# Optimization experiments

Hardware: AMD Instinct MI355X
Metric: run time of the kernel (lower is better)

Reference implementation:

```python
import jax, jax.numpy as jnp
import numpy as np

K = 9  # 3x3 kernel taps

def _conv3x3(x, w, b):
    # standard 3x3 conv, stride 1, pad 1, NCHW
    y = jax.lax.conv_general_dilated(x, w, (1, 1), [(1, 1), (1, 1)],
                                     dimension_numbers=('NCHW', 'OIHW', 'NCHW'))
    return y + b[None, :, None, None]

def setup_inputs() -> dict:
    key = jax.random.key(0)
    ks = jax.random.split(key, 4)
    B, C, Cout, H, W = 2, 256, 256, 128, 128
    x = jax.random.normal(ks[0], (B, C, H, W), jnp.float32)
    w_off = jax.random.normal(ks[1], (3 * K, C, 3, 3), jnp.float32) * 0.01
    b_off = jnp.zeros((3 * K,), jnp.float32)
    weight = jax.random.normal(ks[2], (Cout, C, 3, 3), jnp.float32) * (1.0 / np.sqrt(K * C))
    bias = jnp.zeros((Cout,), jnp.float32)
    gamma = jnp.ones((Cout,), jnp.float32)
    beta = jnp.zeros((Cout,), jnp.float32)
    return {"x": x, "w_off": w_off, "b_off": b_off, "weight": weight,
            "bias": bias, "gamma": gamma, "beta": beta}

def _deform_gather(x, off_y, off_x, mask):
    # x: [B,C,H,W]; off_y/off_x/mask: [B,K,H,W]
    # returns modulated bilinear samples [B,C,K,H,W]
    B, C, H, W = x.shape
    kh = (jnp.arange(K, dtype=x.dtype) // 3).reshape(1, K, 1, 1)
    kw = (jnp.arange(K, dtype=x.dtype) % 3).reshape(1, K, 1, 1)
    # sampling position per tap: base - pad + tap*dilation + learned offset
    py = jnp.arange(H, dtype=x.dtype).reshape(1, 1, H, 1) - 1.0 + kh + off_y
    px = jnp.arange(W, dtype=x.dtype).reshape(1, 1, 1, W) - 1.0 + kw + off_x
    y0 = jnp.floor(py); x0 = jnp.floor(px)
    wy1 = py - y0; wx1 = px - x0
    xf = x.reshape(B, C, H * W)
    def corner(iy, ix, wgt):
        valid = (iy >= 0) & (iy <= H - 1) & (ix >= 0) & (ix <= W - 1)
        iyc = jnp.clip(iy, 0, H - 1).astype(jnp.int32)
        ixc = jnp.clip(ix, 0, W - 1).astype(jnp.int32)
        lin = (iyc * W + ixc).reshape(B, 1, K * H * W)
        g = jnp.take_along_axis(xf, lin, axis=2).reshape(B, C, K, H, W)
        return g * jnp.where(valid, wgt, 0.0)[:, None]  # zero outside borders
    val = (corner(y0,     x0,     (1 - wy1) * (1 - wx1))
         + corner(y0,     x0 + 1, (1 - wy1) * wx1)
         + corner(y0 + 1, x0,     wy1 * (1 - wx1))
         + corner(y0 + 1, x0 + 1, wy1 * wx1))
    return val * mask[:, None]

def reference(x, w_off, b_off, weight, bias, gamma, beta):
    B, C, H, W = x.shape
    om = _conv3x3(x, w_off, b_off)  # [B, 3K, H, W]
    off_y = om[:, :K]
    off_x = om[:, K:2 * K]
    m = jax.nn.sigmoid(om[:, 2 * K:])  # modulation mask
    sampled = _deform_gather(x, off_y, off_x, m)  # [B,C,K,H,W]
    Cout = weight.shape[0]
    y = jnp.einsum('bckhw,ock->bohw', sampled, weight.reshape(Cout, C, K))
    y = y + bias[None, :, None, None]
    # BatchNorm2d (training-mode batch stats, eps=1e-5) + ReLU
    mu = jnp.mean(y, axis=(0, 2, 3), keepdims=True)
    var = jnp.var(y, axis=(0, 2, 3), keepdims=True)
    yn = (y - mu) * jax.lax.rsqrt(var + 1e-5)
    return jax.nn.relu(yn * gamma[None, :, None, None] + beta[None, :, None, None])
```

## Files before the change

kernel.cpp:

```cpp
#include <hip/hip_runtime.h>
#include <hip/hip_fp16.h>
#include <math.h>

#define HW 16384
#define Cc 256
#define CO 256

typedef unsigned short u16;
typedef unsigned int   u32;
typedef __attribute__((ext_vector_type(8))) _Float16 f16x8;
typedef __attribute__((ext_vector_type(4))) float f32x4;

__device__ __forceinline__ u16 f2h(float f) {
    return __half_as_ushort(__float2half(f));
}

__global__ void k_prep(const float* __restrict__ w, const float* __restrict__ wof,
                       u16* __restrict__ wfr, u16* __restrict__ wofr) {
    int id = blockIdx.x * 256 + threadIdx.x;
    if (id < 589824) {
        int i    = id & 7;
        int lane = (id >> 3) & 63;
        int fb   = id >> 9;
        int k32  = fb % 72;
        int ot   = fb / 72;
        int o  = ot * 16 + (lane & 15);
        int K  = k32 * 32 + (lane >> 4) * 8 + i;
        int kt = K >> 8;
        int c  = K & 255;
        wfr[id] = f2h(w[((size_t)o * 256 + c) * 9 + kt]);
    } else if (id < 663552) {
        int id2  = id - 589824;
        int i    = id2 & 7;
        int lane = (id2 >> 3) & 63;
        int fb   = id2 >> 9;
        int k32  = fb % 72;
        int mt   = fb / 72;
        int o  = mt * 16 + (lane & 15);
        int K  = k32 * 32 + (lane >> 4) * 8 + i;
        int t  = K >> 8;
        int c  = K & 255;
        float v = (o < 27) ? wof[((size_t)o * 256 + c) * 9 + t] : 0.0f;
        wofr[id2] = f2h(v);
    }
}

__global__ __launch_bounds__(256) void k_xt(const float* __restrict__ x, u16* __restrict__ Xt) {
    const int tid = threadIdx.x;
    const int bid = blockIdx.x;
    const int hw0 = (bid & 255) * 64;
    const int b   = bid >> 8;
    const int hwl = tid & 63;
    const int cg  = tid >> 6;
    const int hw  = hw0 + hwl;
    const float* xb = x + ((size_t)b << 22);
    u16* dst = Xt + (((size_t)b << 14) + hw) * 256 + cg * 64;
    #pragma unroll
    for (int oct = 0; oct < 8; ++oct) {
        int c0 = cg * 64 + oct * 8;
        u32 pk[4];
        #pragma unroll
        for (int q = 0; q < 4; ++q) {
            float v0 = xb[((size_t)(c0 + 2 * q) << 14) + hw];
            float v1 = xb[((size_t)(c0 + 2 * q + 1) << 14) + hw];
            pk[q] = (u32)f2h(v0) | ((u32)f2h(v1) << 16);
        }
        *(uint4*)(dst + oct * 8) = make_uint4(pk[0], pk[1], pk[2], pk[3]);
    }
}

__global__ __launch_bounds__(256) void k_offmfma(const u16* __restrict__ Xt,
                                                 const u16* __restrict__ wofr,
                                                 const float* __restrict__ bof,
                                                 float* __restrict__ om) {
    const int tid  = threadIdx.x;
    const int wid  = tid >> 6;
    const int lane = tid & 63;
    const int bid  = blockIdx.x;
    const int wq   = bid & 1;
    const int h    = (bid >> 1) & 127;
    const int b    = bid >> 8;

    const int lr = lane & 15;
    const int lg = lane >> 4;
    const int w  = wq * 64 + wid * 16 + lr;

    f32x4 acc0 = (f32x4)0.0f, acc1 = (f32x4)0.0f;
    const u16* XtB = Xt + (((size_t)b << 14) << 8);

    for (int t = 0; t < 9; ++t) {
        int dh = t / 3 - 1;
        int dw = t % 3 - 1;
        int hh = h + dh;
        int ww = w + dw;
        bool valid = (hh >= 0) && (hh < 128) && (ww >= 0) && (ww < 128);
        int hc = min(max(hh, 0), 127);
        int wc = min(max(ww, 0), 127);
        const u16* xrow = XtB + ((size_t)(hc * 128 + wc) << 8) + lg * 8;
        #pragma unroll
        for (int c32 = 0; c32 < 8; ++c32) {
            int k32 = t * 8 + c32;
            f16x8 bv = *(const f16x8*)(xrow + c32 * 32);
            if (!valid) bv = (f16x8)0;
            f16x8 a0 = *(const f16x8*)(wofr + (((size_t)k32 * 64 + lane) << 3));
            f16x8 a1 = *(const f16x8*)(wofr + ((((size_t)(72 + k32)) * 64 + lane) << 3));
            acc0 = __builtin_amdgcn_mfma_f32_16x16x32_f16(a0, bv, acc0, 0, 0, 0);
            acc1 = __builtin_amdgcn_mfma_f32_16x16x32_f16(a1, bv, acc1, 0, 0, 0);
        }
    }

    float* omb = om + ((size_t)b * 27 << 14) + h * 128 + w;
    #pragma unroll
    for (int j = 0; j < 4; ++j) {
        int o = lg * 4 + j;
        omb[(size_t)o << 14] = acc0[j] + bof[o];
        int o1 = 16 + lg * 4 + j;
        if (o1 < 27) omb[(size_t)o1 << 14] = acc1[j] + bof[o1];
    }
}

__global__ __launch_bounds__(512) void k_sgemm(const u16* __restrict__ Xt,
                                               const float* __restrict__ om,
                                               const u16* __restrict__ wfr,
                                               const float* __restrict__ bias,
                                               u16* __restrict__ y,
                                               float* __restrict__ psum) {
    __shared__ int4    soff[9][64];
    __shared__ __half2 swt2[9][64][4];
    __shared__ __align__(16) u16 Blds[2][4096];

    const int tid  = threadIdx.x;
    const int wid  = tid >> 6;
    const int lane = tid & 63;
    const int bid  = ((blockIdx.x & 7) << 6) | (blockIdx.x >> 3);
    const int p0   = bid * 64;
    const int b    = p0 >> 14;
    const int hwb  = p0 & 16383;

    for (int e = tid; e < 576; e += 512) {
        int t = e >> 6, j = e & 63;
        int hw = hwb + j;
        int h = hw >> 7, wc = hw & 127;
        const size_t ob = (size_t)b * 27 * HW;
        float oy = om[ob + (size_t)t * HW + hw];
        float ox = om[ob + (size_t)(9 + t) * HW + hw];
        float mv = om[ob + (size_t)(18 + t) * HW + hw];
        mv = 1.0f / (1.0f + expf(-mv));
        float py = (float)h - 1.0f + (float)(t / 3) + oy;
        float px = (float)wc - 1.0f + (float)(t % 3) + ox;
        float y0f = floorf(py), x0f = floorf(px);
        float wy = py - y0f, wx = px - x0f;
        int iy = (int)y0f, ix = (int)x0f;
        float w4[4] = {(1.0f - wy) * (1.0f - wx), (1.0f - wy) * wx,
                       wy * (1.0f - wx),          wy * wx};
        const int dy[4] = {0, 0, 1, 1};
        const int dx[4] = {0, 1, 0, 1};
        int of[4];
        #pragma unroll
        for (int r = 0; r < 4; ++r) {
            int yy = iy + dy[r], xx = ix + dx[r];
            bool v = (yy >= 0) && (yy <= 127) && (xx >= 0) && (xx <= 127);
            int yc = min(max(yy, 0), 127);
            int xc = min(max(xx, 0), 127);
            of[r] = yc * 128 + xc;
            swt2[t][j][r] = __float2half2_rn(v ? w4[r] * mv : 0.0f);
        }
        soff[t][j] = make_int4(of[0], of[1], of[2], of[3]);
    }
    __syncthreads();

    const int jp    = tid >> 3;
    const int kloc8 = (((tid & 7) ^ (jp & 7)) << 3);
    const u16* XtB  = Xt + (((size_t)b << 14) << 8);

    const int lg = lane >> 4;
    const int lr = lane & 15;

    f32x4 acc[2][4];
    #pragma unroll
    for (int m = 0; m < 2; ++m)
        #pragma unroll
        for (int n = 0; n < 4; ++n) acc[m][n] = (f32x4)0.0f;

    auto gload = [&](int s, uint4* gg) {
        int t = s >> 2;
        int c = ((s & 3) << 6) + kloc8;
        int4 oa = soff[t][jp];
        gg[0] = *(const uint4*)(XtB + (size_t)oa.x * 256 + c);
        gg[1] = *(const uint4*)(XtB + (size_t)oa.y * 256 + c);
        gg[2] = *(const uint4*)(XtB + (size_t)oa.z * 256 + c);
        gg[3] = *(const uint4*)(XtB + (size_t)oa.w * 256 + c);
    };
    auto gcomb = [&](int s, const uint4* gg, int buf) {
        int t = s >> 2;
        __half2 w0 = swt2[t][jp][0];
        __half2 w1 = swt2[t][jp][1];
        __half2 w2 = swt2[t][jp][2];
        __half2 w3 = swt2[t][jp][3];
        const __half2* c0 = (const __half2*)&gg[0];
        const __half2* c1 = (const __half2*)&gg[1];
        const __half2* c2 = (const __half2*)&gg[2];
        const __half2* c3 = (const __half2*)&gg[3];
        u32 o4[4];
        #pragma unroll
        for (int q = 0; q < 4; ++q) {
            __half2 o = __hmul2(c0[q], w0);
            o = __hfma2(c1[q], w1, o);
            o = __hfma2(c2[q], w2, o);
            o = __hfma2(c3[q], w3, o);
            o4[q] = *(const u32*)&o;
        }
        *(uint4*)((char*)&Blds[buf][0] + tid * 16) = make_uint4(o4[0], o4[1], o4[2], o4[3]);
    };
    auto aload = [&](int k32g, f16x8 dst2[2][2]) {
        #pragma unroll
        for (int kk = 0; kk < 2; ++kk)
            #pragma unroll
            for (int m = 0; m < 2; ++m)
                dst2[kk][m] = *(const f16x8*)(wfr +
                    ((size_t)((wid * 2 + m) * 72 + k32g + kk) << 9) + (size_t)lane * 8);
    };

    f16x8 af[2][2];
    {
        uint4 g[4];
        gload(0, g);
        aload(0, af);
        gcomb(0, g, 0);
    }
    __syncthreads();

    int cur = 0;
    for (int s = 0; s < 36; ++s) {
        const int nxt = cur ^ 1;
        uint4 gn[4];
        f16x8 afn[2][2];
        if (s < 35) {
            gload(s + 1, gn);
            aload(2 * (s + 1), afn);
        }

        const char* bb2 = (const char*)&Blds[cur][0];
        #pragma unroll
        for (int kk = 0; kk < 2; ++kk) {
            f16x8 bfv[4];
            #pragma unroll
            for (int n = 0; n < 4; ++n) {
                int row  = n * 16 + lr;
                int boff = row * 128 + ((kk * 64 + lg * 16) ^ ((row & 7) << 4));
                bfv[n] = *(const f16x8*)(bb2 + boff);
            }
            #pragma unroll
            for (int m = 0; m < 2; ++m)
                #pragma unroll
                for (int n = 0; n < 4; ++n)
                    acc[m][n] = __builtin_amdgcn_mfma_f32_16x16x32_f16(af[kk][m], bfv[n], acc[m][n], 0, 0, 0);
        }

        if (s < 35) {
            gcomb(s + 1, gn, nxt);
            #pragma unroll
            for (int kk = 0; kk < 2; ++kk)
                #pragma unroll
                for (int m = 0; m < 2; ++m)
                    af[kk][m] = afn[kk][m];
        }
        __syncthreads();
        cur = nxt;
    }

    const int hw0  = hwb + lr;
    const int slot = (bid & 31) << 9;
    #pragma unroll
    for (int m = 0; m < 2; ++m) {
        #pragma unroll
        for (int jj = 0; jj < 4; ++jj) {
            int o = wid * 32 + m * 16 + lg * 4 + jj;
            float bv = bias[o];
            u16* ya = y + ((size_t)b * 256 + o) * HW + hw0;
            float ssum = 0.0f, ssq = 0.0f;
            #pragma unroll
            for (int n = 0; n < 4; ++n) {
                float v = acc[m][n][jj] + bv;
                ya[n * 16] = f2h(v);
                ssum += v;
                ssq  += v * v;
            }
            #pragma unroll
            for (int d = 1; d < 16; d <<= 1) {
                ssum += __shfl_xor(ssum, d);
                ssq  += __shfl_xor(ssq, d);
            }
            if (lr == 0) {
                atomicAdd(&psum[slot + o], ssum);
                atomicAdd(&psum[slot + 256 + o], ssq);
            }
        }
    }
}

__global__ void k_stats2(const float* __restrict__ psum, float* __restrict__ st) {
    int o = threadIdx.x;
    float s = 0.0f, q = 0.0f;
    #pragma unroll 8
    for (int r = 0; r < 32; ++r) {
        s += psum[(r << 9) + o];
        q += psum[(r << 9) + 256 + o];
    }
    float mu  = s / 32768.0f;
    float var = q / 32768.0f - mu * mu;
    st[o]       = mu;
    st[256 + o] = rsqrtf(var + 1e-5f);
}

__global__ void k_norm(const u16* __restrict__ y, const float* __restrict__ stats,
                       const float* __restrict__ gamma, const float* __restrict__ beta,
                       float* __restrict__ out) {
    int i8 = blockIdx.x * 256 + threadIdx.x;
    if (i8 >= (2 * CO * HW) / 8) return;
    int o = ((i8 * 8) >> 14) & 255;
    float g  = gamma[o] * stats[256 + o];
    float bt = beta[o] - stats[o] * g;
    uint4 v = ((const uint4*)y)[i8];
    const __half2* h2 = (const __half2*)&v;
    float4 r0, r1;
    float2 f0 = __half22float2(h2[0]);
    float2 f1 = __half22float2(h2[1]);
    float2 f2 = __half22float2(h2[2]);
    float2 f3 = __half22float2(h2[3]);
    r0.x = fmaxf(fmaf(f0.x, g, bt), 0.0f);
    r0.y = fmaxf(fmaf(f0.y, g, bt), 0.0f);
    r0.z = fmaxf(fmaf(f1.x, g, bt), 0.0f);
    r0.w = fmaxf(fmaf(f1.y, g, bt), 0.0f);
    r1.x = fmaxf(fmaf(f2.x, g, bt), 0.0f);
    r1.y = fmaxf(fmaf(f2.y, g, bt), 0.0f);
    r1.z = fmaxf(fmaf(f3.x, g, bt), 0.0f);
    r1.w = fmaxf(fmaf(f3.y, g, bt), 0.0f);
    float4* op = (float4*)(out + (size_t)i8 * 8);
    op[0] = r0;
    op[1] = r1;
}

extern "C" void kernel_launch(void* const* d_in, const int* in_sizes, int n_in,
                              void* d_out, int out_size, void* d_ws, size_t ws_size,
                              hipStream_t stream) {
    const float* x      = (const float*)d_in[0];
    const float* w_off  = (const float*)d_in[1];
    const float* b_off  = (const float*)d_in[2];
    const float* weight = (const float*)d_in[3];
    const float* bias   = (const float*)d_in[4];
    const float* gamma  = (const float*)d_in[5];
    const float* beta   = (const float*)d_in[6];
    float* out = (float*)d_out;

    float* ws   = (float*)d_ws;
    float* om   = ws;
    float* st   = om + 884736;
    float* ps   = st + 512;
    u16*   yb   = (u16*)(ps + 16384);
    u16*   wfr  = yb + 8388608;
    u16*   wofr = wfr + 589824;
    u16*   Xt   = wofr + 73728;

    k_prep<<<2592, 256, 0, stream>>>(weight, w_off, wfr, wofr);
    k_xt<<<512, 256, 0, stream>>>(x, Xt);
    hipMemsetAsync(ps, 0, 16384 * sizeof(float), stream);
    k_offmfma<<<512, 256, 0, stream>>>(Xt, wofr, b_off, om);

    k_sgemm<<<512, 512, 0, stream>>>(Xt, om, wfr, bias, yb, ps);

    k_stats2<<<1, 256, 0, stream>>>(ps, st);
    k_norm<<<(2 * CO * HW / 8 + 255) / 256, 256, 0, stream>>>(yb, st, gamma, beta, out);
}
```

Baseline: 123.4 us.

## Fuse prep kernels and double K-step per stage in deformable GEMM

Merges the weight reordering, input transpose and partial-sum zeroing into one launch, dropping two launches and a memset. In the main deformable GEMM, each pipeline stage now covers 128 channels instead of 64. That halves the loop trip count and barriers and doubles in-flight gathers per thread, with a wider LDS swizzle. The cost is more registers and twice the LDS for the B buffers, which may reduce occupancy.

```diff
diff --git a/kernel.cpp b/kernel.cpp
--- a/kernel.cpp
+++ b/kernel.cpp
@@ -15,57 +15,63 @@
     return __half_as_ushort(__float2half(f));
 }
 
-__global__ void k_prep(const float* __restrict__ w, const float* __restrict__ wof,
-                       u16* __restrict__ wfr, u16* __restrict__ wofr) {
-    int id = blockIdx.x * 256 + threadIdx.x;
-    if (id < 589824) {
-        int i    = id & 7;
-        int lane = (id >> 3) & 63;
-        int fb   = id >> 9;
-        int k32  = fb % 72;
-        int ot   = fb / 72;
-        int o  = ot * 16 + (lane & 15);
-        int K  = k32 * 32 + (lane >> 4) * 8 + i;
-        int kt = K >> 8;
-        int c  = K & 255;
-        wfr[id] = f2h(w[((size_t)o * 256 + c) * 9 + kt]);
-    } else if (id < 663552) {
-        int id2  = id - 589824;
-        int i    = id2 & 7;
-        int lane = (id2 >> 3) & 63;
-        int fb   = id2 >> 9;
-        int k32  = fb % 72;
-        int mt   = fb / 72;
-        int o  = mt * 16 + (lane & 15);
-        int K  = k32 * 32 + (lane >> 4) * 8 + i;
-        int t  = K >> 8;
-        int c  = K & 255;
-        float v = (o < 27) ? wof[((size_t)o * 256 + c) * 9 + t] : 0.0f;
-        wofr[id2] = f2h(v);
-    }
-}
-
-__global__ __launch_bounds__(256) void k_xt(const float* __restrict__ x, u16* __restrict__ Xt) {
+__global__ __launch_bounds__(256) void k_prep(const float* __restrict__ x,
+                                              const float* __restrict__ w,
+                                              const float* __restrict__ wof,
+                                              u16* __restrict__ wfr, u16* __restrict__ wofr,
+                                              u16* __restrict__ Xt, float* __restrict__ ps) {
+    const int blk = blockIdx.x;
     const int tid = threadIdx.x;
-    const int bid = blockIdx.x;
-    const int hw0 = (bid & 255) * 64;
-    const int b   = bid >> 8;
-    const int hwl = tid & 63;
-    const int cg  = tid >> 6;
-    const int hw  = hw0 + hwl;
-    const float* xb = x + ((size_t)b << 22);
-    u16* dst = Xt + (((size_t)b << 14) + hw) * 256 + cg * 64;
-    #pragma unroll
-    for (int oct = 0; oct < 8; ++oct) {
-        int c0 = cg * 64 + oct * 8;
-        u32 pk[4];
-        #pragma unroll
-        for (int q = 0; q < 4; ++q) {
-            float v0 = xb[((size_t)(c0 + 2 * q) << 14) + hw];
-            float v1 = xb[((size_t)(c0 + 2 * q + 1) << 14) + hw];
-            pk[q] = (u32)f2h(v0) | ((u32)f2h(v1) << 16);
-        }
-        *(uint4*)(dst + oct * 8) = make_uint4(pk[0], pk[1], pk[2], pk[3]);
+    if (blk < 512) {
+        const int hw0 = (blk & 255) * 64;
+        const int b   = blk >> 8;
+        const int hwl = tid & 63;
+        const int cg  = tid >> 6;
+        const int hw  = hw0 + hwl;
+        const float* xb = x + ((size_t)b << 22);
+        u16* dst = Xt + (((size_t)b << 14) + hw) * 256 + cg * 64;
+        #pragma unroll
+        for (int oct = 0; oct < 8; ++oct) {
+            int c0 = cg * 64 + oct * 8;
+            u32 pk[4];
+            #pragma unroll
+            for (int q = 0; q < 4; ++q) {
+                float v0 = xb[((size_t)(c0 + 2 * q) << 14) + hw];
+                float v1 = xb[((size_t)(c0 + 2 * q + 1) << 14) + hw];
+                pk[q] = (u32)f2h(v0) | ((u32)f2h(v1) << 16);
+            }
+            *(uint4*)(dst + oct * 8) = make_uint4(pk[0], pk[1], pk[2], pk[3]);
+        }
+    } else if (blk < 3104) {
+        int id = (blk - 512) * 256 + tid;
+        if (id < 589824) {
+            int i    = id & 7;
+            int lane = (id >> 3) & 63;
+            int fb   = id >> 9;
+            int k32  = fb % 72;
+            int ot   = fb / 72;
+            int o  = ot * 16 + (lane & 15);
+            int K  = k32 * 32 + (lane >> 4) * 8 + i;
+            int kt = K >> 8;
+            int c  = K & 255;
+            wfr[id] = f2h(w[((size_t)o * 256 + c) * 9 + kt]);
+        } else if (id < 663552) {
+            int id2  = id - 589824;
+            int i    = id2 & 7;
+            int lane = (id2 >> 3) & 63;
+            int fb   = id2 >> 9;
+            int k32  = fb % 72;
+            int mt   = fb / 72;
+            int o  = mt * 16 + (lane & 15);
+            int K  = k32 * 32 + (lane >> 4) * 8 + i;
+            int t  = K >> 8;
+            int c  = K & 255;
+            float v = (o < 27) ? wof[((size_t)o * 256 + c) * 9 + t] : 0.0f;
+            wofr[id2] = f2h(v);
+        }
+    } else {
+        int id3 = (blk - 3104) * 256 + tid;
+        if (id3 < 16384) ps[id3] = 0.0f;
     }
 }
 
@@ -127,7 +133,7 @@
                                                float* __restrict__ psum) {
     __shared__ int4    soff[9][64];
     __shared__ __half2 swt2[9][64][4];
-    __shared__ __align__(16) u16 Blds[2][4096];
+    __shared__ __align__(16) u16 Blds[2][8192];
 
     const int tid  = threadIdx.x;
     const int wid  = tid >> 6;
@@ -169,8 +175,11 @@
     }
     __syncthreads();
 
-    const int jp    = tid >> 3;
-    const int kloc8 = (((tid & 7) ^ (jp & 7)) << 3);
+    const int jp  = tid >> 3;
+    const int sw  = jp & 15;
+    const int q0  = (tid & 7) << 1;
+    const int kloc0 = ((q0 ^ sw) << 3);
+    const int kloc1 = (((q0 | 1) ^ sw) << 3);
     const u16* XtB  = Xt + (((size_t)b << 14) << 8);
 
     const int lg = lane >> 4;
@@ -183,47 +192,59 @@
         for (int n = 0; n < 4; ++n) acc[m][n] = (f32x4)0.0f;
 
     auto gload = [&](int s, uint4* gg) {
-        int t = s >> 2;
-        int c = ((s & 3) << 6) + kloc8;
+        int t = s >> 1;
+        int cb = (s & 1) << 7;
         int4 oa = soff[t][jp];
-        gg[0] = *(const uint4*)(XtB + (size_t)oa.x * 256 + c);
-        gg[1] = *(const uint4*)(XtB + (size_t)oa.y * 256 + c);
-        gg[2] = *(const uint4*)(XtB + (size_t)oa.z * 256 + c);
-        gg[3] = *(const uint4*)(XtB + (size_t)oa.w * 256 + c);
+        const u16* pa = XtB + (size_t)oa.x * 256 + cb;
+        const u16* pb = XtB + (size_t)oa.y * 256 + cb;
+        const u16* pc = XtB + (size_t)oa.z * 256 + cb;
+        const u16* pd = XtB + (size_t)oa.w * 256 + cb;
+        gg[0] = *(const uint4*)(pa + kloc0);
+        gg[1] = *(const uint4*)(pb + kloc0);
+        gg[2] = *(const uint4*)(pc + kloc0);
+        gg[3] = *(const uint4*)(pd + kloc0);
+        gg[4] = *(const uint4*)(pa + kloc1);
+        gg[5] = *(const uint4*)(pb + kloc1);
+        gg[6] = *(const uint4*)(pc + kloc1);
+        gg[7] = *(const uint4*)(pd + kloc1);
     };
     auto gcomb = [&](int s, const uint4* gg, int buf) {
-        int t = s >> 2;
+        int t = s >> 1;
         __half2 w0 = swt2[t][jp][0];
         __half2 w1 = swt2[t][jp][1];
         __half2 w2 = swt2[t][jp][2];
         __half2 w3 = swt2[t][jp][3];
-        const __half2* c0 = (const __half2*)&gg[0];
-        const __half2* c1 = (const __half2*)&gg[1];
-        const __half2* c2 = (const __half2*)&gg[2];
-        const __half2* c3 = (const __half2*)&gg[3];
-        u32 o4[4];
+        const __half2* hh = (const __half2*)gg;
+        u32 oA[4], oB[4];
         #pragma unroll
         for (int q = 0; q < 4; ++q) {
-            __half2 o = __hmul2(c0[q], w0);
-            o = __hfma2(c1[q], w1, o);
-            o = __hfma2(c2[q], w2, o);
-            o = __hfma2(c3[q], w3, o);
-            o4[q] = *(const u32*)&o;
-        }
-        *(uint4*)((char*)&Blds[buf][0] + tid * 16) = make_uint4(o4[0], o4[1], o4[2], o4[3]);
+            __half2 o = __hmul2(hh[q], w0);
+            o = __hfma2(hh[4 + q],  w1, o);
+            o = __hfma2(hh[8 + q],  w2, o);
+            o = __hfma2(hh[12 + q], w3, o);
+            oA[q] = *(const u32*)&o;
+            __half2 o2 = __hmul2(hh[16 + q], w0);
+            o2 = __hfma2(hh[20 + q], w1, o2);
+            o2 = __hfma2(hh[24 + q], w2, o2);
+            o2 = __hfma2(hh[28 + q], w3, o2);
+            oB[q] = *(const u32*)&o2;
+        }
+        char* dst = (char*)&Blds[buf][0] + tid * 32;
+        *(uint4*)dst        = make_uint4(oA[0], oA[1], oA[2], oA[3]);
+        *(uint4*)(dst + 16) = make_uint4(oB[0], oB[1], oB[2], oB[3]);
     };
-    auto aload = [&](int k32g, f16x8 dst2[2][2]) {
-        #pragma unroll
-        for (int kk = 0; kk < 2; ++kk)
+    auto aload = [&](int k32g, f16x8 dst2[4][2]) {
+        #pragma unroll
+        for (int kk = 0; kk < 4; ++kk)
             #pragma unroll
             for (int m = 0; m < 2; ++m)
                 dst2[kk][m] = *(const f16x8*)(wfr +
                     ((size_t)((wid * 2 + m) * 72 + k32g + kk) << 9) + (size_t)lane * 8);
     };
 
-    f16x8 af[2][2];
+    f16x8 af[4][2];
     {
-        uint4 g[4];
+        uint4 g[8];
         gload(0, g);
         aload(0, af);
         gcomb(0, g, 0);
@@ -231,23 +252,23 @@
     __syncthreads();
 
     int cur = 0;
-    for (int s = 0; s < 36; ++s) {
+    for (int s = 0; s < 18; ++s) {
         const int nxt = cur ^ 1;
-        uint4 gn[4];
-        f16x8 afn[2][2];
-        if (s < 35) {
+        uint4 gn[8];
+        f16x8 afn[4][2];
+        if (s < 17) {
             gload(s + 1, gn);
-            aload(2 * (s + 1), afn);
+            aload(4 * (s + 1), afn);
         }
 
         const char* bb2 = (const char*)&Blds[cur][0];
         #pragma unroll
-        for (int kk = 0; kk < 2; ++kk) {
+        for (int kk = 0; kk < 4; ++kk) {
             f16x8 bfv[4];
             #pragma unroll
             for (int n = 0; n < 4; ++n) {
                 int row  = n * 16 + lr;
-                int boff = row * 128 + ((kk * 64 + lg * 16) ^ ((row & 7) << 4));
+                int boff = row * 256 + ((((kk * 4 + lg) ^ (row & 15))) << 4);
                 bfv[n] = *(const f16x8*)(bb2 + boff);
             }
             #pragma unroll
@@ -257,10 +278,10 @@
                     acc[m][n] = __builtin_amdgcn_mfma_f32_16x16x32_f16(af[kk][m], bfv[n], acc[m][n], 0, 0, 0);
         }
 
-        if (s < 35) {
+        if (s < 17) {
             gcomb(s + 1, gn, nxt);
             #pragma unroll
-            for (int kk = 0; kk < 2; ++kk)
+            for (int kk = 0; kk < 4; ++kk)
                 #pragma unroll
                 for (int m = 0; m < 2; ++m)
                     af[kk][m] = afn[kk][m];
@@ -362,9 +383,7 @@
     u16*   wofr = wfr + 589824;
     u16*   Xt   = wofr + 73728;
 
-    k_prep<<<2592, 256, 0, stream>>>(weight, w_off, wfr, wofr);
-    k_xt<<<512, 256, 0, stream>>>(x, Xt);
-    hipMemsetAsync(ps, 0, 16384 * sizeof(float), stream);
+    k_prep<<<3168, 256, 0, stream>>>(x, weight, w_off, wfr, wofr, Xt, ps);
     k_offmfma<<<512, 256, 0, stream>>>(Xt, wofr, b_off, om);
 
     k_sgemm<<<512, 512, 0, stream>>>(Xt, om, wfr, bias, yb, ps);
```

After: 122.3 us. No clear change (-0.9%).
